# Performance work log

Measured on AMD Instinct MI355X. Metric: run time of the kernel, lower is better.

The kernel has to match this reference:

```python
import jax, jax.numpy as jnp
import numpy as np

EPSILON = float(np.finfo(np.float32).tiny)
K = 32                 # self.k
TRAIN_ENSEMBLE = 2     # repeat_sample in train mode
TAU = 0.1


def setup_inputs() -> dict:
    key = jax.random.key(0)
    scores = jax.random.normal(key, (256, 8192, 4), dtype=jnp.float32)  # [bsz, Nmax, ensemble]
    return {"scores": scores}


def reference(scores):
    bsz, Nmax, ensemble = scores.shape
    repeat = TRAIN_ENSEMBLE
    local_k = min(K, Nmax)

    # flat_scores: (bsz*ensemble, Nmax), then repeated over samples -> (repeat*bsz*ensemble, Nmax)
    flat = scores.transpose(0, 2, 1).reshape(bsz * ensemble, Nmax)
    flat = jnp.tile(flat, (repeat, 1))

    # Gumbel(0,1) noise (m.sample())
    g = jax.random.gumbel(jax.random.key(42), flat.shape, dtype=flat.dtype)
    flat = flat + g

    zeros = jnp.zeros_like(flat)

    def step(carry, _):
        f, khot, onehot = carry
        khot_mask = jnp.maximum(1.0 - onehot, EPSILON)
        f = f + jnp.log(khot_mask)
        onehot = jax.nn.softmax(f / TAU, axis=1)
        return (f, khot + onehot, onehot), None

    (_, khot, _), _ = jax.lax.scan(step, (flat, zeros, zeros), None, length=local_k)

    # hard top-k straight-through
    _, ind = jax.lax.top_k(khot, local_k)                      # (R, local_k)
    rows = jnp.arange(khot.shape[0])[:, None]
    khot_hard = jnp.zeros_like(khot).at[rows, ind].set(1.0)
    res = khot_hard - jax.lax.stop_gradient(khot) + khot

    # (repeat, bsz, ensemble, Nmax) -> (repeat, bsz, Nmax, ensemble)
    new_mask = res.reshape(repeat, bsz, ensemble, Nmax).transpose(0, 1, 3, 2)
    return new_mask
```

## Files before the change

### kernel.cpp

```cpp
#include <hip/hip_runtime.h>

#define TPB 256
#define ROWN 8192
#define CMAX 1024
#define EPS_TINY 1.1754943508222875e-38f

__device__ __forceinline__ unsigned rotl32(unsigned x, int r) {
  return (x << r) | (x >> (32 - r));
}

__device__ __forceinline__ unsigned tf_pxor(unsigned idx) {
  const unsigned ks0 = 0u, ks1 = 42u, ks2 = 0x1BD11BDAu ^ 0u ^ 42u;
  unsigned x0 = ks0;
  unsigned x1 = idx + ks1;
#define TF4(a,b,cc,d) \
  x0 += x1; x1 = rotl32(x1,(a));  x1 ^= x0; \
  x0 += x1; x1 = rotl32(x1,(b));  x1 ^= x0; \
  x0 += x1; x1 = rotl32(x1,(cc)); x1 ^= x0; \
  x0 += x1; x1 = rotl32(x1,(d));  x1 ^= x0;
  TF4(13,15,26,6)   x0 += ks1; x1 += ks2 + 1u;
  TF4(17,29,16,24)  x0 += ks2; x1 += ks0 + 2u;
  TF4(13,15,26,6)   x0 += ks0; x1 += ks1 + 3u;
  TF4(17,29,16,24)  x0 += ks1; x1 += ks2 + 4u;
  TF4(13,15,26,6)   x0 += ks2; x1 += ks0 + 5u;
#undef TF4
  return x0 ^ x1;
}

__device__ __forceinline__ float gumbel_of(unsigned idx) {
  const unsigned bits = tf_pxor(idx);
  float u = __uint_as_float((bits >> 9) | 0x3f800000u) - 1.0f;
  u = u + EPS_TINY;
  u = fmaxf(EPS_TINY, u);
  return -logf(-logf(u));
}

__device__ __forceinline__ float approx_gumbel(unsigned bits) {
  float u = __uint_as_float((bits >> 9) | 0x3f800000u) - 1.0f;
  u = u + EPS_TINY;
  u = fmaxf(EPS_TINY, u);
  float t;
  if (u >= 0.75f) {
    const float v = 1.0f - u;
    t = v * (1.0f + v * (0.5f + v * (0.33333334f + v * (0.25f + v * 0.2f))));
  } else {
    t = -0.69314718f * __log2f(u);
  }
  return -0.69314718f * __log2f(t);
}

__device__ __forceinline__ unsigned key16_of(float x) {
  const unsigned b = __float_as_uint(x) >> 16;
  return (b & 0x8000u) ? (0xFFFFu & ~b) : (b | 0x8000u);
}

__global__ __launch_bounds__(TPB, 8)
void topk_row(const void* __restrict__ scores_raw, int* __restrict__ selws) {
  const int t    = threadIdx.x;
  const int lane = t & 63;
  const int wave = t >> 6;

  const int i   = blockIdx.x;
  const int xcd = i & 7;
  const int k   = i >> 3;
  const int e   = k & 3;
  const int q   = k >> 2;
  const int b   = xcd * 32 + (q & 31);
  const int rep = q >> 5;
  const int r   = rep * 1024 + b * 4 + e;
  const unsigned gbase = (unsigned)r * (unsigned)ROWN;

  __shared__ unsigned       kLds[16][TPB];
  __shared__ unsigned short candIdx[CMAX];
  __shared__ float redM[4];
  __shared__ float redZ[2][4];
  __shared__ int   wtot[13][4];
  __shared__ int   f32flag;

  if (t == 0) f32flag = 0;
  __syncthreads();
  {
    const unsigned* w = (const unsigned*)scores_raw;
    bool bad = false;
#pragma unroll
    for (int p = 0; p < 4; ++p) {
      const unsigned x = w[t + 256 * p];
      const float flo = __uint_as_float((x & 0xFFFFu) << 16);
      const float fhi = __uint_as_float(x & 0xFFFF0000u);
      if (!(fabsf(flo) <= 16.0f) || !(fabsf(fhi) <= 16.0f)) bad = true;
    }
    if (bad) f32flag = 1;
  }
  __syncthreads();
  const bool in_f32 = (f32flag != 0);

  const size_t ebase0 = ((size_t)b * ROWN + (size_t)t) * 4 + (size_t)e;
  float m = -3.4e38f;
  {
    unsigned pair = 0u;
    if (in_f32) {
      const float* sp = (const float*)scores_raw;
#pragma unroll
      for (int j = 0; j < 32; ++j) {
        const float fj = sp[ebase0 + (size_t)(256 * j) * 4]
                       + approx_gumbel(tf_pxor(gbase + (unsigned)(t + 256 * j)));
        m = fmaxf(m, fj);
        const unsigned kk = key16_of(fj);
        if (j & 1) { pair |= kk << 16; kLds[j >> 1][t] = pair; }
        else pair = kk;
      }
    } else {
      const unsigned short* sp = (const unsigned short*)scores_raw;
#pragma unroll
      for (int j = 0; j < 32; ++j) {
        const float fj = __uint_as_float(((unsigned)sp[ebase0 + (size_t)(256 * j) * 4]) << 16)
                       + approx_gumbel(tf_pxor(gbase + (unsigned)(t + 256 * j)));
        m = fmaxf(m, fj);
        const unsigned kk = key16_of(fj);
        if (j & 1) { pair |= kk << 16; kLds[j >> 1][t] = pair; }
        else pair = kk;
      }
    }
  }

#pragma unroll
  for (int off = 32; off >= 1; off >>= 1) m = fmaxf(m, __shfl_xor(m, off));
  if (lane == 0) redM[wave] = m;
  __syncthreads();
  m = fmaxf(fmaxf(redM[0], redM[1]), fmaxf(redM[2], redM[3]));

  float lo = m - 25.0f, hi = m;
#pragma unroll 1
  for (int itb = 0; itb < 12; ++itb) {
    const float mid = 0.5f * (lo + hi);
    const unsigned kmid = key16_of(mid);
    int c = 0;
#pragma unroll
    for (int h = 0; h < 16; ++h) {
      const unsigned w = kLds[h][t];
      c += ((w & 0xFFFFu) > kmid) ? 1 : 0;
      c += ((w >> 16) > kmid) ? 1 : 0;
    }
#pragma unroll
    for (int off = 32; off >= 1; off >>= 1) c += __shfl_xor(c, off);
    if (lane == 0) wtot[itb][wave] = c;
    __syncthreads();
    const int tot = wtot[itb][0] + wtot[itb][1] + wtot[itb][2] + wtot[itb][3];
    if (tot >= 33) lo = mid; else hi = mid;
  }
  const float theta = lo - 2.34f;
  const unsigned ktheta = key16_of(theta);

  int cj = 0;
#pragma unroll
  for (int h = 0; h < 16; ++h) {
    const unsigned w = kLds[h][t];
    cj += ((w & 0xFFFFu) >= ktheta) ? 1 : 0;
    cj += ((w >> 16) >= ktheta) ? 1 : 0;
  }
  int incv = cj;
#pragma unroll
  for (int off = 1; off < 64; off <<= 1) {
    const int v = __shfl_up(incv, off);
    if (lane >= off) incv += v;
  }
  if (lane == 63) wtot[12][wave] = incv;
  __syncthreads();
  int base = 0;
  for (int w = 0; w < wave; ++w) base += wtot[12][w];
  int cnt = wtot[12][0] + wtot[12][1] + wtot[12][2] + wtot[12][3];
  if (cnt > CMAX) cnt = CMAX;
  int o = base + incv - cj;
#pragma unroll
  for (int h = 0; h < 16; ++h) {
    const unsigned w = kLds[h][t];
    if ((w & 0xFFFFu) >= ktheta) {
      if (o < CMAX) candIdx[o] = (unsigned short)(t + 256 * (2 * h));
      ++o;
    }
    if ((w >> 16) >= ktheta) {
      if (o < CMAX) candIdx[o] = (unsigned short)(t + 256 * (2 * h + 1));
      ++o;
    }
  }
  __syncthreads();

  float cfr[4], khr[4];
#pragma unroll
  for (int p = 0; p < 4; ++p) {
    cfr[p] = -3.0e38f; khr[p] = -3.0e38f;
    if (256 * p < cnt) {
      const int ci = t + 256 * p;
      if (ci < cnt) {
        const int n = (int)candIdx[ci];
        const size_t ei = ((size_t)b * ROWN + (size_t)n) * 4 + (size_t)e;
        float sc;
        if (in_f32) sc = ((const float*)scores_raw)[ei];
        else sc = __uint_as_float(((unsigned)((const unsigned short*)scores_raw)[ei]) << 16);
        cfr[p] = sc + gumbel_of(gbase + (unsigned)n);
        khr[p] = 0.0f;
      }
    }
  }

  float m2 = 0.0f;
#pragma unroll 1
  for (int it = 0; it < 32; ++it) {
    if ((it & 3) == 0) {
      float mm = -3.4e38f;
#pragma unroll
      for (int p = 0; p < 4; ++p)
        if (256 * p < cnt) mm = fmaxf(mm, cfr[p]);
#pragma unroll
      for (int off = 32; off >= 1; off >>= 1) mm = fmaxf(mm, __shfl_xor(mm, off));
      if (lane == 0) redM[wave] = mm;
      __syncthreads();
      m2 = fmaxf(fmaxf(redM[0], redM[1]), fmaxf(redM[2], redM[3]));
    }

    float ek[4];
    float Z = 0.0f;
#pragma unroll
    for (int p = 0; p < 4; ++p) {
      float ev = 0.0f;
      if (256 * p < cnt) {
        ev = __expf((cfr[p] - m2) * 10.0f);
        Z += ev;
      }
      ek[p] = ev;
    }
#pragma unroll
    for (int off = 32; off >= 1; off >>= 1) Z += __shfl_xor(Z, off);
    if (lane == 0) redZ[it & 1][wave] = Z;
    __syncthreads();
    Z = (redZ[it & 1][0] + redZ[it & 1][1]) + (redZ[it & 1][2] + redZ[it & 1][3]);

    const float rz = __builtin_amdgcn_rcpf(Z);
#pragma unroll
    for (int p = 0; p < 4; ++p) {
      if (256 * p < cnt) {
        const float pp = ek[p] * rz;
        khr[p] += pp;
        cfr[p] += __logf(fmaxf(1.0f - pp, EPS_TINY));
      }
    }
  }

  float* khLds = (float*)&kLds[0][0];
#pragma unroll
  for (int p = 0; p < 4; ++p) {
    if (256 * p < cnt) {
      const int ci = t + 256 * p;
      if (ci < cnt) khLds[ci] = khr[p];
    }
  }
  __syncthreads();
  if (wave != 0) return;

  const int nch = (cnt + 63) >> 6;
#pragma unroll 1
  for (int pass = 0; pass < 32; ++pass) {
    float bv = -3.4e38f; int bn = 0x7FFFFFFF; int bci = 0;
#pragma unroll 1
    for (int c = 0; c < nch; ++c) {
      const int ci = lane + 64 * c;
      if (ci < cnt) {
        const float v = khLds[ci];
        const int  n = (int)candIdx[ci];
        if (v > bv || (v == bv && n < bn)) { bv = v; bn = n; bci = ci; }
      }
    }
#pragma unroll
    for (int off = 32; off >= 1; off >>= 1) {
      const float ov = __shfl_xor(bv, off);
      const int   on = __shfl_xor(bn, off);
      const int   oc = __shfl_xor(bci, off);
      if (ov > bv || (ov == bv && on < bn)) { bv = ov; bn = on; bci = oc; }
    }
    if (lane == 0) {
      selws[r * 32 + pass] = bn;
      khLds[bci] = -3.0e38f;
    }
  }
}

__global__ __launch_bounds__(TPB)
void expand_out(const int* __restrict__ selws, float4* __restrict__ out4) {
  const int t   = threadIdx.x;
  const int blk = blockIdx.x;
  const int grp = blk >> 2;
  const int s   = blk & 3;
  const int rep = grp >> 8;
  const int b   = grp & 255;

  __shared__ unsigned ebm[4 * 256];
#pragma unroll
  for (int p = 0; p < 4; ++p) ebm[t + 256 * p] = 0u;
  __syncthreads();
  if (t < 4) {
    const int r = rep * 1024 + b * 4 + t;
#pragma unroll 1
    for (int p = 0; p < 32; ++p) {
      const int ix = selws[r * 32 + p];
      ebm[t * 256 + (ix >> 5)] |= (1u << (ix & 31));
    }
  }
  __syncthreads();

  const size_t obase = (size_t)grp * ROWN;
#pragma unroll
  for (int j = 0; j < 8; ++j) {
    const int n = s * 2048 + t + 256 * j;
    float4 v;
    v.x = ((ebm[0 * 256 + (n >> 5)] >> (n & 31)) & 1u) ? 1.0f : 0.0f;
    v.y = ((ebm[1 * 256 + (n >> 5)] >> (n & 31)) & 1u) ? 1.0f : 0.0f;
    v.z = ((ebm[2 * 256 + (n >> 5)] >> (n & 31)) & 1u) ? 1.0f : 0.0f;
    v.w = ((ebm[3 * 256 + (n >> 5)] >> (n & 31)) & 1u) ? 1.0f : 0.0f;
    out4[obase + (size_t)n] = v;
  }
}

extern "C" void kernel_launch(void* const* d_in, const int* in_sizes, int n_in,
                              void* d_out, int out_size, void* d_ws, size_t ws_size,
                              hipStream_t stream) {
  const void* scores = d_in[0];
  int* selws = (int*)d_ws;
  topk_row<<<dim3(2048), dim3(TPB), 0, stream>>>(scores, selws);
  expand_out<<<dim3(2048), dim3(TPB), 0, stream>>>(selws, (float4*)d_out);
}
```

Baseline: 231.5 us.

## Merge max-refresh barrier into softmax sum barrier and shorten threshold bisection

The periodic max reduction in the 32-step softmax loop now runs in the same barrier as the Z sum, using double-buffered shared slots, so the separate refresh __syncthreads per four iterations goes away. The max is taken from pre-update logits and applied one step later, which is still a safe upper bound because the logits only decrease. The threshold bisection is also cut from 12 to 7 iterations, giving a coarser cutoff that can admit more candidates into the later stages.

New measurement: 227.9 us. About the same (-1.5%).

```diff
diff --git a/kernel.cpp b/kernel.cpp
--- a/kernel.cpp
+++ b/kernel.cpp
@@ -72,7 +72,7 @@
 
   __shared__ unsigned       kLds[16][TPB];
   __shared__ unsigned short candIdx[CMAX];
-  __shared__ float redM[4];
+  __shared__ float redM[2][4];
   __shared__ float redZ[2][4];
   __shared__ int   wtot[13][4];
   __shared__ int   f32flag;
@@ -125,13 +125,13 @@
 
 #pragma unroll
   for (int off = 32; off >= 1; off >>= 1) m = fmaxf(m, __shfl_xor(m, off));
-  if (lane == 0) redM[wave] = m;
-  __syncthreads();
-  m = fmaxf(fmaxf(redM[0], redM[1]), fmaxf(redM[2], redM[3]));
+  if (lane == 0) redM[0][wave] = m;
+  __syncthreads();
+  m = fmaxf(fmaxf(redM[0][0], redM[0][1]), fmaxf(redM[0][2], redM[0][3]));
 
   float lo = m - 25.0f, hi = m;
 #pragma unroll 1
-  for (int itb = 0; itb < 12; ++itb) {
+  for (int itb = 0; itb < 7; ++itb) {
     const float mid = 0.5f * (lo + hi);
     const unsigned kmid = key16_of(mid);
     int c = 0;
@@ -203,21 +203,21 @@
     }
   }
 
-  float m2 = 0.0f;
+  float m2;
+  {
+    float mm = -3.4e38f;
+#pragma unroll
+    for (int p = 0; p < 4; ++p)
+      if (256 * p < cnt) mm = fmaxf(mm, cfr[p]);
+#pragma unroll
+    for (int off = 32; off >= 1; off >>= 1) mm = fmaxf(mm, __shfl_xor(mm, off));
+    if (lane == 0) redM[1][wave] = mm;
+    __syncthreads();
+    m2 = fmaxf(fmaxf(redM[1][0], redM[1][1]), fmaxf(redM[1][2], redM[1][3]));
+  }
+
 #pragma unroll 1
   for (int it = 0; it < 32; ++it) {
-    if ((it & 3) == 0) {
-      float mm = -3.4e38f;
-#pragma unroll
-      for (int p = 0; p < 4; ++p)
-        if (256 * p < cnt) mm = fmaxf(mm, cfr[p]);
-#pragma unroll
-      for (int off = 32; off >= 1; off >>= 1) mm = fmaxf(mm, __shfl_xor(mm, off));
-      if (lane == 0) redM[wave] = mm;
-      __syncthreads();
-      m2 = fmaxf(fmaxf(redM[0], redM[1]), fmaxf(redM[2], redM[3]));
-    }
-
     float ek[4];
     float Z = 0.0f;
 #pragma unroll
@@ -232,8 +232,24 @@
 #pragma unroll
     for (int off = 32; off >= 1; off >>= 1) Z += __shfl_xor(Z, off);
     if (lane == 0) redZ[it & 1][wave] = Z;
+
+    const bool refresh = ((it & 3) == 2);
+    if (refresh) {
+      float mm = -3.4e38f;
+#pragma unroll
+      for (int p = 0; p < 4; ++p)
+        if (256 * p < cnt) mm = fmaxf(mm, cfr[p]);
+#pragma unroll
+      for (int off = 32; off >= 1; off >>= 1) mm = fmaxf(mm, __shfl_xor(mm, off));
+      if (lane == 0) redM[(it >> 2) & 1][wave] = mm;
+    }
     __syncthreads();
     Z = (redZ[it & 1][0] + redZ[it & 1][1]) + (redZ[it & 1][2] + redZ[it & 1][3]);
+    float m2n = m2;
+    if (refresh) {
+      const int bm = (it >> 2) & 1;
+      m2n = fmaxf(fmaxf(redM[bm][0], redM[bm][1]), fmaxf(redM[bm][2], redM[bm][3]));
+    }
 
     const float rz = __builtin_amdgcn_rcpf(Z);
 #pragma unroll
@@ -244,6 +260,7 @@
         cfr[p] += __logf(fmaxf(1.0f - pp, EPS_TINY));
       }
     }
+    m2 = m2n;
   }
 
   float* khLds = (float*)&kLds[0][0];
```
